# Kernel optimization log

Measured on AMD Instinct MI355X. Metric: run time of the kernel, lower is better.

The kernel has to match this reference:

```python
import jax, jax.numpy as jnp
import numpy as np

B, S, D, H, O, E, K = 8, 2048, 768, 3072, 768, 8, 2
LN_EPS = 1e-5


def setup_inputs() -> dict:
    key = jax.random.key(0)
    ks = jax.random.split(key, 8)
    x = jax.random.normal(ks[0], (B, S, D), dtype=jnp.float32)
    router_w = jax.random.normal(ks[1], (D, E), dtype=jnp.float32) * 0.02
    router_b = jnp.zeros((E,), dtype=jnp.float32)
    w1 = jax.random.normal(ks[2], (E, D, H), dtype=jnp.float32) * 0.02
    b1 = jnp.zeros((E, H), dtype=jnp.float32)
    w2 = jax.random.normal(ks[3], (E, H, O), dtype=jnp.float32) * 0.02
    b2 = jnp.zeros((E, O), dtype=jnp.float32)
    ln_g = jnp.ones((O,), dtype=jnp.float32)
    ln_b = jnp.zeros((O,), dtype=jnp.float32)
    return {"x": x, "router_w": router_w, "router_b": router_b,
            "w1": w1, "b1": b1, "w2": w2, "b2": b2,
            "ln_g": ln_g, "ln_b": ln_b}


def _layernorm(y, g, b):
    mu = jnp.mean(y, axis=-1, keepdims=True)
    var = jnp.mean(jnp.square(y - mu), axis=-1, keepdims=True)
    return (y - mu) * jax.lax.rsqrt(var + LN_EPS) * g + b


def reference(x, router_w, router_b, w1, b1, w2, b2, ln_g, ln_b):
    # Router (NoisyTopKRouter, eval mode: no noise): top-k gate over expert logits
    logits = jnp.einsum('bsd,de->bse', x, router_w) + router_b   # [B,S,E]
    top_vals, top_idx = jax.lax.top_k(logits, K)                 # [B,S,K]
    routing_weights = jax.nn.softmax(top_vals, axis=-1)          # [B,S,K]

    out = jnp.zeros((B, S, O), dtype=x.dtype)
    for e in range(E):
        # per-token combined weight for this expert (0 if not routed)
        w_e = jnp.sum(routing_weights * (top_idx == e), axis=-1)  # [B,S]
        # dense per-expert feedforward on ALL tokens (as in original loop)
        h = jax.nn.gelu(jnp.einsum('bsd,dh->bsh', x, w1[e]) + b1[e])
        y = jnp.einsum('bsh,ho->bso', h, w2[e]) + b2[e]
        out = out + y * w_e[..., None]
    return _layernorm(out, ln_g, ln_b)
```

## Files before the change

### kernel.cpp

```cpp
#include <hip/hip_runtime.h>
#include <hip/hip_bf16.h>
#include <stdint.h>

#define Bq  8
#define Sq  2048
#define Dq  768
#define Hq  3072
#define Oq  768
#define Eq  8
#define Mq  (Bq*Sq)
#define LN_EPS 1e-5f
#define MAX_TILES (2*Mq/128 + 16)

typedef unsigned short u16;
typedef __attribute__((ext_vector_type(4))) float f32x4;
typedef __attribute__((ext_vector_type(8))) __bf16 bf16x8;

static __device__ __forceinline__ u16 f2bf(float f) {
  __hip_bfloat16 h = __float2bfloat16(f);
  return __builtin_bit_cast(u16, h);
}

static __device__ __forceinline__ float gelu_f(float x) {
  float u = 0.7978845608028654f * x * (1.0f + 0.044715f * x * x);
  float e = __expf(2.0f * u);
  float t = 1.0f - 2.0f / (e + 1.0f);
  return 0.5f * x * (1.0f + t);
}

typedef const __attribute__((address_space(1))) void* gas_t;
typedef __attribute__((address_space(3))) void* las_t;
static __device__ __forceinline__ void gload16(const void* g, void* l) {
  __builtin_amdgcn_global_load_lds((gas_t)g, (las_t)l, 16, 0, 0);
}

__global__ __launch_bounds__(256) void router_cvt_kernel(
    const float* __restrict__ x, const float* __restrict__ rw,
    const float* __restrict__ rb, u16* __restrict__ Xbf,
    int* __restrict__ tok_seg, float2* __restrict__ tok_w)
{
  __shared__ float rwT[Eq * Dq];
  for (int i = threadIdx.x; i < Eq * Dq; i += 256)
    rwT[(i & 7) * Dq + (i >> 3)] = rw[i];
  __syncthreads();

  int wid = threadIdx.x >> 6;
  int lane = threadIdx.x & 63;
  int token = blockIdx.x * 4 + wid;
  const float4* xrow = (const float4*)(x + (size_t)token * Dq);
  ushort4* orow = (ushort4*)(Xbf + (size_t)token * Dq);

  float acc[Eq];
#pragma unroll
  for (int e = 0; e < Eq; e++) acc[e] = 0.f;

#pragma unroll
  for (int it = 0; it < Dq / 256; it++) {
    int d4 = it * 64 + lane;
    float4 xv = xrow[d4];
    ushort4 o;
    o.x = f2bf(xv.x); o.y = f2bf(xv.y); o.z = f2bf(xv.z); o.w = f2bf(xv.w);
    orow[d4] = o;
    int d = d4 * 4;
#pragma unroll
    for (int e = 0; e < Eq; e++) {
      float4 wv = *(const float4*)&rwT[e * Dq + d];
      acc[e] += xv.x * wv.x + xv.y * wv.y + xv.z * wv.z + xv.w * wv.w;
    }
  }
#pragma unroll
  for (int e = 0; e < Eq; e++) {
    float v = acc[e];
#pragma unroll
    for (int off = 32; off; off >>= 1) v += __shfl_xor(v, off);
    acc[e] = v;
  }
  if (lane == 0) {
    float v1 = -1e30f, v2 = -1e30f; int i1 = 0, i2 = 0;
#pragma unroll
    for (int e = 0; e < Eq; e++) {
      float v = acc[e] + rb[e];
      if (v > v1)      { v2 = v1; i2 = i1; v1 = v; i1 = e; }
      else if (v > v2) { v2 = v;  i2 = e; }
    }
    float ex = expf(v2 - v1);
    float wa = 1.f / (1.f + ex);
    float wb = ex / (1.f + ex);
    tok_seg[token] = i1 | ((8 + i2) << 8);
    tok_w[token] = make_float2(wa, wb);
  }
}

__global__ __launch_bounds__(256) void scatter_build(
    const int* __restrict__ tok_seg, const float2* __restrict__ tok_w,
    int* __restrict__ cnt, int* __restrict__ seg_tok, float* __restrict__ seg_wgt)
{
  __shared__ int histA[16], histB[16], base[16];
  int t = threadIdx.x;
  if (t < 16) { histA[t] = 0; histB[t] = 0; }
  __syncthreads();
  int token = blockIdx.x * 256 + t;
  int sp = tok_seg[token];
  float2 wv = tok_w[token];
  int s0 = sp & 0xff, s1 = sp >> 8;
  atomicAdd(&histA[s0], 1);
  atomicAdd(&histA[s1], 1);
  __syncthreads();
  if (t < 16) base[t] = atomicAdd(&cnt[t], histA[t]);
  __syncthreads();
  int p0 = base[s0] + atomicAdd(&histB[s0], 1);
  seg_tok[(size_t)s0 * Mq + p0] = token;
  seg_wgt[(size_t)s0 * Mq + p0] = wv.x;
  int p1 = base[s1] + atomicAdd(&histB[s1], 1);
  seg_tok[(size_t)s1 * Mq + p1] = token;
  seg_wgt[(size_t)s1 * Mq + p1] = wv.y;
}

__global__ void prefix_kernel(const int* __restrict__ cnt, int* __restrict__ prefix)
{
  if (threadIdx.x == 0 && blockIdx.x == 0) {
    int t = 0;
#pragma unroll
    for (int s = 0; s < 16; s++) { prefix[s] = t; t += (cnt[s] + 127) >> 7; }
    prefix[16] = t;
  }
}

__global__ __launch_bounds__(256) void transpose_cvt(
    const float* __restrict__ in, u16* __restrict__ out, int R, int C)
{
  __shared__ float tile[32][33];
  int e = blockIdx.z;
  in  += (size_t)e * R * C;
  out += (size_t)e * R * C;
  int c0 = blockIdx.x * 32, r0 = blockIdx.y * 32;
  int tx = threadIdx.x & 31, ty = threadIdx.x >> 5;
#pragma unroll
  for (int rr = 0; rr < 32; rr += 8)
    tile[rr + ty][tx] = in[(size_t)(r0 + rr + ty) * C + c0 + tx];
  __syncthreads();
#pragma unroll
  for (int rr = 0; rr < 32; rr += 8)
    out[(size_t)(c0 + rr + ty) * R + r0 + tx] = f2bf(tile[tx][rr + ty]);
}

template<int EPI>
__global__ __launch_bounds__(512, 4) void moe_gemm(
    const u16* __restrict__ A, const u16* __restrict__ W,
    const float* __restrict__ bias,
    u16* __restrict__ Hout, float* __restrict__ out,
    const int* __restrict__ cnt, const int* __restrict__ prefix,
    const int* __restrict__ seg_tok, const float* __restrict__ seg_wgt,
    int K, int N, int tile_lo)
{
  const int NP = N / 256;
  const int lid = (int)blockIdx.x + NP * (int)blockIdx.y;
  const int xcd = lid & 7, slot = lid >> 3;
  const int t_loc = xcd + 8 * (slot / NP);
  const int panel = slot % NP;

  const int t = tile_lo + t_loc;
  const int total = prefix[16];
  if (t >= total) return;
  int seg = 0;
#pragma unroll
  for (int s = 1; s < 16; s++) if (prefix[s] <= t) seg = s;
  const int e = seg & 7;
  const int segcnt = cnt[seg];
  const int ti = t - prefix[seg];
  const int lt = t_loc;

  __shared__ u16 As[2][128 * 32];
  __shared__ u16 Bs[2][256 * 32];
  const int tid  = threadIdx.x;
  const int lane = tid & 63;
  const int wid  = tid >> 6;
  const int wr   = wid >> 2, wc = wid & 3;
  const int lrow = lane & 15, kgrp = lane >> 4;
  const int kx   = kgrp ^ ((lrow >> 1) & 3);
  const int n0 = panel * 256;

  f32x4 acc[4][4];
#pragma unroll
  for (int m = 0; m < 4; m++)
#pragma unroll
    for (int n = 0; n < 4; n++) acc[m][n] = (f32x4){0.f, 0.f, 0.f, 0.f};

  const int r0 = tid >> 2;
  const int kc = (((tid & 3) ^ ((tid >> 3) & 3)) * 8);
  const u16 *gA0;
  if (EPI == 0) {
    int i0 = ti * 128 + r0;
    int tok0 = (i0 < segcnt) ? seg_tok[(size_t)seg * Mq + i0] : 0;
    gA0 = A + (size_t)tok0 * K + kc;
  } else {
    gA0 = A + (size_t)(lt * 128 + r0) * K + kc;
  }
  const u16* gB = W + (size_t)e * K * N + (size_t)(n0 + r0) * K + kc;
  const size_t rowskipB = (size_t)128 * K;
  const int lofs = tid * 8;

  auto stage = [&](int b) {
    gload16(gA0, &As[b][lofs]);
    gload16(gB,            &Bs[b][lofs]);
    gload16(gB + rowskipB, &Bs[b][lofs + 4096]);
    gA0 += 32; gB += 32;
  };

  const int NIT = K / 32;
  stage(0);
  for (int it = 0; it < NIT; ++it) {
    const int cur = it & 1;
    if (it + 1 < NIT) {
      stage(cur ^ 1);
      asm volatile("s_waitcnt vmcnt(3)" ::: "memory");
    } else {
      asm volatile("s_waitcnt vmcnt(0)" ::: "memory");
    }
    __builtin_amdgcn_s_barrier();
    __builtin_amdgcn_sched_barrier(0);
    bf16x8 a[4], b[4];
#pragma unroll
    for (int m = 0; m < 4; m++)
      a[m] = *(const bf16x8*)&As[cur][(wr * 64 + m * 16 + lrow) * 32 + kx * 8];
#pragma unroll
    for (int n = 0; n < 4; n++)
      b[n] = *(const bf16x8*)&Bs[cur][(wc * 64 + n * 16 + lrow) * 32 + kx * 8];
#pragma unroll
    for (int m = 0; m < 4; m++)
#pragma unroll
      for (int n = 0; n < 4; n++)
        acc[m][n] = __builtin_amdgcn_mfma_f32_16x16x32_bf16(a[m], b[n], acc[m][n], 0, 0, 0);
    __builtin_amdgcn_sched_barrier(0);
    __builtin_amdgcn_s_barrier();
  }

  const int rbase = wr * 64;
  const int cbase = n0 + wc * 64;
  if (EPI == 0) {
#pragma unroll
    for (int n = 0; n < 4; n++) {
      int c = cbase + n * 16 + lrow;
      float bv = bias[(size_t)e * N + c];
#pragma unroll
      for (int m = 0; m < 4; m++)
#pragma unroll
        for (int j = 0; j < 4; j++) {
          int r = rbase + m * 16 + kgrp * 4 + j;
          float v = acc[m][n][j] + bv;
          Hout[(size_t)(lt * 128 + r) * N + c] = f2bf(gelu_f(v));
        }
    }
  } else {
#pragma unroll
    for (int m = 0; m < 4; m++)
#pragma unroll
      for (int j = 0; j < 4; j++) {
        int r = rbase + m * 16 + kgrp * 4 + j;
        int i = ti * 128 + r;
        if (i < segcnt) {
          int token = seg_tok[(size_t)seg * Mq + i];
          float w = seg_wgt[(size_t)seg * Mq + i];
          float* orow = out + (size_t)token * Oq;
#pragma unroll
          for (int n = 0; n < 4; n++) {
            int c = cbase + n * 16 + lrow;
            float v = (acc[m][n][j] + bias[(size_t)e * N + c]) * w;
            unsafeAtomicAdd(&orow[c], v);
          }
        }
      }
  }
}

__global__ __launch_bounds__(256) void ln_kernel(
    float* __restrict__ io, const float* __restrict__ g, const float* __restrict__ b)
{
  int wid = threadIdx.x >> 6, lane = threadIdx.x & 63;
  int row = blockIdx.x * 4 + wid;
  float* p = io + (size_t)row * Oq;
  float v[Oq / 64];
  float s = 0.f;
#pragma unroll
  for (int i = 0; i < Oq / 64; i++) { v[i] = p[lane + i * 64]; s += v[i]; }
#pragma unroll
  for (int off = 32; off; off >>= 1) s += __shfl_xor(s, off);
  float mu = s * (1.0f / Oq);
  float q = 0.f;
#pragma unroll
  for (int i = 0; i < Oq / 64; i++) { float d = v[i] - mu; q += d * d; }
#pragma unroll
  for (int off = 32; off; off >>= 1) q += __shfl_xor(q, off);
  float inv = rsqrtf(q * (1.0f / Oq) + LN_EPS);
#pragma unroll
  for (int i = 0; i < Oq / 64; i++) {
    int c = lane + i * 64;
    p[c] = (v[i] - mu) * inv * g[c] + b[c];
  }
}

extern "C" void kernel_launch(void* const* d_in, const int* in_sizes, int n_in,
                              void* d_out, int out_size, void* d_ws, size_t ws_size,
                              hipStream_t stream)
{
  const float* x    = (const float*)d_in[0];
  const float* rw   = (const float*)d_in[1];
  const float* rb   = (const float*)d_in[2];
  const float* w1   = (const float*)d_in[3];
  const float* b1   = (const float*)d_in[4];
  const float* w2   = (const float*)d_in[5];
  const float* b2   = (const float*)d_in[6];
  const float* ln_g = (const float*)d_in[7];
  const float* ln_b = (const float*)d_in[8];
  float* out = (float*)d_out;

  char* ws = (char*)d_ws;
  size_t off = 0;
  auto alloc = [&](size_t bytes) {
    void* p = ws + off;
    off += (bytes + 255) & ~(size_t)255;
    return p;
  };
  int*    cnt     = (int*)alloc(16 * 4);
  int*    prefix  = (int*)alloc(17 * 4);
  int*    tok_seg = (int*)alloc((size_t)Mq * 4);
  float2* tok_w   = (float2*)alloc((size_t)Mq * 8);
  int*    seg_tok = (int*)alloc((size_t)16 * Mq * 4);
  float*  seg_wgt = (float*)alloc((size_t)16 * Mq * 4);
  u16* Xbf = (u16*)alloc((size_t)Mq * Dq * 2);
  u16* W1T = (u16*)alloc((size_t)Eq * Dq * Hq * 2);
  u16* W2T = (u16*)alloc((size_t)Eq * Hq * Oq * 2);

  size_t remain = (ws_size > off) ? ws_size - off : 0;
  size_t tile_bytes = (size_t)128 * Hq * 2;
  long long wt = (long long)(remain / tile_bytes);
  if (wt > MAX_TILES) wt = MAX_TILES;
  wt &= ~7LL;
  if (wt < 8) wt = 8;
  int WT = (int)wt;
  u16* Hbuf = (u16*)alloc((size_t)WT * tile_bytes);

  hipMemsetAsync(out, 0, (size_t)Mq * Oq * 4, stream);
  hipMemsetAsync(cnt, 0, 16 * 4, stream);
  router_cvt_kernel<<<Mq / 4, 256, 0, stream>>>(x, rw, rb, Xbf, tok_seg, tok_w);
  scatter_build<<<Mq / 256, 256, 0, stream>>>(tok_seg, tok_w, cnt, seg_tok, seg_wgt);
  prefix_kernel<<<1, 64, 0, stream>>>(cnt, prefix);
  transpose_cvt<<<dim3(Hq / 32, Dq / 32, Eq), 256, 0, stream>>>(w1, W1T, Dq, Hq);
  transpose_cvt<<<dim3(Oq / 32, Hq / 32, Eq), 256, 0, stream>>>(w2, W2T, Hq, Oq);

  for (int tl = 0; tl < MAX_TILES; tl += WT) {
    int gx = MAX_TILES - tl; if (gx > WT) gx = WT;
    moe_gemm<0><<<dim3(Hq / 256, gx), 512, 0, stream>>>(
        Xbf, W1T, b1, Hbuf, nullptr, cnt, prefix, seg_tok, seg_wgt,
        Dq, Hq, tl);
    moe_gemm<1><<<dim3(Oq / 256, gx), 512, 0, stream>>>(
        Hbuf, W2T, b2, nullptr, out, cnt, prefix, seg_tok, seg_wgt,
        Hq, Oq, tl);
  }
  ln_kernel<<<Mq / 4, 256, 0, stream>>>(out, ln_g, ln_b);
}
```

Measured before the change: 748.1 us.

## Deepen MoE GEMM LDS pipeline to four stages with one barrier per step

Replaces the double-buffered K loop with a four-buffer ring, keeping three 32-wide K slices of global loads in flight and issuing the next stage after the LDS fragment reads. This drops one of the two barriers per iteration and raises wave priority around the MFMA block so that memory latency is hidden better. LDS use per block doubles to 96 KB and the occupancy hint in launch_bounds is removed, so fewer blocks can be resident per CU.

```diff
diff --git a/kernel.cpp b/kernel.cpp
--- a/kernel.cpp
+++ b/kernel.cpp
@@ -145,7 +145,7 @@
 }
 
 template<int EPI>
-__global__ __launch_bounds__(512, 4) void moe_gemm(
+__global__ __launch_bounds__(512) void moe_gemm(
     const u16* __restrict__ A, const u16* __restrict__ W,
     const float* __restrict__ bias,
     u16* __restrict__ Hout, float* __restrict__ out,
@@ -170,8 +170,8 @@
   const int ti = t - prefix[seg];
   const int lt = t_loc;
 
-  __shared__ u16 As[2][128 * 32];
-  __shared__ u16 Bs[2][256 * 32];
+  __shared__ u16 As[4][128 * 32];
+  __shared__ u16 Bs[4][256 * 32];
   const int tid  = threadIdx.x;
   const int lane = tid & 63;
   const int wid  = tid >> 6;
@@ -207,33 +207,44 @@
     gA0 += 32; gB += 32;
   };
 
-  const int NIT = K / 32;
-  stage(0);
-  for (int it = 0; it < NIT; ++it) {
-    const int cur = it & 1;
-    if (it + 1 < NIT) {
-      stage(cur ^ 1);
+  auto phase = [&](int p, int vm) {
+    const int buf = p & 3;
+    bf16x8 a[4], b[4];
+#pragma unroll
+    for (int m = 0; m < 4; m++)
+      a[m] = *(const bf16x8*)&As[buf][(wr * 64 + m * 16 + lrow) * 32 + kx * 8];
+#pragma unroll
+    for (int n = 0; n < 4; n++)
+      b[n] = *(const bf16x8*)&Bs[buf][(wc * 64 + n * 16 + lrow) * 32 + kx * 8];
+    if (vm == 6) {
+      stage((p + 3) & 3);
+      asm volatile("s_waitcnt vmcnt(6)" ::: "memory");
+    } else if (vm == 3) {
       asm volatile("s_waitcnt vmcnt(3)" ::: "memory");
-    } else {
+    } else if (vm == 0) {
       asm volatile("s_waitcnt vmcnt(0)" ::: "memory");
     }
-    __builtin_amdgcn_s_barrier();
     __builtin_amdgcn_sched_barrier(0);
-    bf16x8 a[4], b[4];
-#pragma unroll
-    for (int m = 0; m < 4; m++)
-      a[m] = *(const bf16x8*)&As[cur][(wr * 64 + m * 16 + lrow) * 32 + kx * 8];
-#pragma unroll
-    for (int n = 0; n < 4; n++)
-      b[n] = *(const bf16x8*)&Bs[cur][(wc * 64 + n * 16 + lrow) * 32 + kx * 8];
+    __builtin_amdgcn_s_setprio(1);
 #pragma unroll
     for (int m = 0; m < 4; m++)
 #pragma unroll
       for (int n = 0; n < 4; n++)
         acc[m][n] = __builtin_amdgcn_mfma_f32_16x16x32_bf16(a[m], b[n], acc[m][n], 0, 0, 0);
+    __builtin_amdgcn_s_setprio(0);
     __builtin_amdgcn_sched_barrier(0);
     __builtin_amdgcn_s_barrier();
-  }
+  };
+
+  const int NPH = K / 32;
+  stage(0); stage(1); stage(2);
+  asm volatile("s_waitcnt vmcnt(6)" ::: "memory");
+  __builtin_amdgcn_s_barrier();
+  int p = 0;
+  for (; p < NPH - 3; ++p) phase(p, 6);
+  phase(p, 3); ++p;
+  phase(p, 0); ++p;
+  phase(p, -1);
 
   const int rbase = wr * 64;
   const int cbase = n0 + wc * 64;
```

New measurement: 785.2 us. +5.0%, slower.
